# Kernel optimization log

Hardware: AMD Instinct MI355X
Metric: run time of the kernel (lower is better)

## Reference

```python
import jax, jax.numpy as jnp
import numpy as np

EMBED = 768
HEADS = 12
HEAD_DIM = EMBED // HEADS


def setup_inputs() -> dict:
    key = jax.random.key(0)
    ks = jax.random.split(key, 7)
    B, S = 4, 2048
    scale = 1.0 / np.sqrt(EMBED)
    return {
        "q": jax.random.normal(ks[0], (B, S, EMBED), dtype=jnp.float32),
        "k": jax.random.normal(ks[1], (B, S, EMBED), dtype=jnp.float32),
        "v": jax.random.normal(ks[2], (B, S, EMBED), dtype=jnp.float32),
        # NOTE: original torch code applies self.query to q, k AND v (bug kept faithfully),
        # so only the query projection and the output projection participate.
        "Wq": (jax.random.normal(ks[3], (EMBED, EMBED), dtype=jnp.float32) * scale),
        "bq": jnp.zeros((EMBED,), dtype=jnp.float32),
        "Wo": (jax.random.normal(ks[4], (EMBED, EMBED), dtype=jnp.float32) * scale),
        "bo": jnp.zeros((EMBED,), dtype=jnp.float32),
    }


def _split_heads(x):
    B, S, _ = x.shape
    return x.reshape(B, S, HEADS, HEAD_DIM).transpose(0, 2, 1, 3)  # [B,H,S,D]


def reference(q, k, v, Wq, bq, Wo, bo):
    # All three streams go through the *query* projection (faithful to source bug).
    qh = _split_heads(q @ Wq.T + bq)
    kh = _split_heads(k @ Wq.T + bq)
    vh = _split_heads(v @ Wq.T + bq)
    scores = jnp.einsum("bhsd,bhtd->bhst", qh, kh) / np.sqrt(HEAD_DIM)  # [B,H,S,S]
    attn = jax.nn.softmax(scores, axis=-1)  # dropout = identity (eval mode)
    out = jnp.einsum("bhst,bhtd->bhsd", attn, vh)  # [B,H,S,D]
    B, H, S, D = out.shape
    out = out.transpose(0, 2, 1, 3).reshape(B, S, H * D)  # [B,S,E]
    return out @ Wo.T + bo
```

## Files before the change

### kernel.cpp

```cpp
#include <hip/hip_runtime.h>

typedef unsigned int  uint32;
typedef unsigned short ushort_t;

using s16x8 = __attribute__((ext_vector_type(8))) short;
using bf8v  = __attribute__((ext_vector_type(8))) __bf16;
using f16x4 = __attribute__((ext_vector_type(4))) _Float16;
using f16x8 = __attribute__((ext_vector_type(8))) _Float16;
using f32x4 = __attribute__((ext_vector_type(4))) float;

typedef __attribute__((address_space(1))) void as1_void;
typedef __attribute__((address_space(3))) void as3_void;

__device__ __forceinline__ void gld16(const void* g, void* l) {
  __builtin_amdgcn_global_load_lds((const as1_void*)g, (as3_void*)l, 16, 0, 0);
}

__device__ __forceinline__ f32x4 mfma32(s16x8 a, s16x8 b, f32x4 c) {
  return __builtin_amdgcn_mfma_f32_16x16x32_bf16(
      __builtin_bit_cast(bf8v, a), __builtin_bit_cast(bf8v, b), c, 0, 0, 0);
}
__device__ __forceinline__ f32x4 mfma32h(f16x8 a, f16x8 b, f32x4 c) {
  return __builtin_amdgcn_mfma_f32_16x16x32_f16(a, b, c, 0, 0, 0);
}

__device__ __forceinline__ ushort_t f2bf(float f) {
  uint32 u = __float_as_uint(f);
  u += 0x7FFFu + ((u >> 16) & 1u);
  return (ushort_t)(u >> 16);
}
__device__ __forceinline__ f16x4 exp_pack(f32x4 st) {
  float e0 = __builtin_amdgcn_exp2f(st[0]);
  float e1 = __builtin_amdgcn_exp2f(st[1]);
  float e2 = __builtin_amdgcn_exp2f(st[2]);
  float e3 = __builtin_amdgcn_exp2f(st[3]);
  uint2 u = {__builtin_bit_cast(uint32, __builtin_amdgcn_cvt_pkrtz(e0, e1)),
             __builtin_bit_cast(uint32, __builtin_amdgcn_cvt_pkrtz(e2, e3))};
  return __builtin_bit_cast(f16x4, u);
}

__global__ __launch_bounds__(256) void cvt_all(const float* __restrict__ q,
                                               const float* __restrict__ k,
                                               const float* __restrict__ v,
                                               const float* __restrict__ Wq,
                                               const float* __restrict__ Wo,
                                               ushort_t* qb, ushort_t* kb, ushort_t* vb,
                                               ushort_t* wqb, ushort_t* wob) {
  int i = blockIdx.x * 256 + threadIdx.x;
  const float* s; ushort_t* d; int off;
  if (i < 4718592) {
    int st = i / 1572864; off = i - st * 1572864;
    s = st == 0 ? q : (st == 1 ? k : v);
    d = st == 0 ? qb : (st == 1 ? kb : vb);
  } else {
    int j = i - 4718592; int st = j / 147456; off = j - st * 147456;
    s = st ? Wo : Wq; d = st ? wob : wqb;
  }
  float4 f = ((const float4*)s)[off];
  ushort4 o = {f2bf(f.x), f2bf(f.y), f2bf(f.z), f2bf(f.w)};
  ((ushort4*)d)[off] = o;
}

__device__ __forceinline__ void gemm_core(const ushort_t* __restrict__ A,
                                          const ushort_t* __restrict__ Bw,
                                          ushort_t* As, ushort_t* Bs,
                                          int m0, int n0, f32x4 (&acc)[4][4]) {
  const int tid = threadIdx.x;
  const int wave = tid >> 6, lane = tid & 63;
  const int qd = lane >> 4, c = lane & 15;
  const int wm = wave >> 1, wn = wave & 1;
  const int pc0 = qd ^ (c & 7), pc1 = (4 + qd) ^ (c & 7);
  int row[4], cl[4], lb[4];
#pragma unroll
  for (int i = 0; i < 4; ++i) {
    int s = i * 256 + wave * 64 + lane;
    row[i] = s >> 3; cl[i] = (s & 7) ^ (row[i] & 7);
    lb[i] = (i * 256 + wave * 64) * 16;
  }
  for (int kt = 0; kt < 12; ++kt) {
    __syncthreads();
#pragma unroll
    for (int i = 0; i < 4; ++i) {
      gld16(A + (size_t)(m0 + row[i]) * 768 + kt * 64 + cl[i] * 8, (char*)As + lb[i]);
      gld16(Bw + (size_t)(n0 + row[i]) * 768 + kt * 64 + cl[i] * 8, (char*)Bs + lb[i]);
    }
    __syncthreads();
#pragma unroll
    for (int kk = 0; kk < 2; ++kk) {
      const int pcr = kk ? pc1 : pc0;
      s16x8 a[4], b[4];
#pragma unroll
      for (int i = 0; i < 4; ++i) a[i] = *(const s16x8*)(As + (wm * 64 + i * 16 + c) * 64 + pcr * 8);
#pragma unroll
      for (int j = 0; j < 4; ++j) b[j] = *(const s16x8*)(Bs + (wn * 64 + j * 16 + c) * 64 + pcr * 8);
#pragma unroll
      for (int i = 0; i < 4; ++i)
#pragma unroll
        for (int j = 0; j < 4; ++j) acc[i][j] = mfma32(a[i], b[j], acc[i][j]);
    }
  }
}

__global__ __launch_bounds__(256) void gemm_proj(const ushort_t* __restrict__ qb,
                                                 const ushort_t* __restrict__ kb,
                                                 const ushort_t* __restrict__ vb,
                                                 const ushort_t* __restrict__ Wqb,
                                                 const float* __restrict__ bias,
                                                 ushort_t* __restrict__ qh,
                                                 ushort_t* __restrict__ kh,
                                                 ushort_t* __restrict__ vt) {
  __shared__ __align__(16) ushort_t As[8192];
  __shared__ __align__(16) ushort_t Bs[8192];
  const int bz = blockIdx.z;
  const ushort_t* A = bz == 0 ? qb : (bz == 1 ? kb : vb);
  const int m0 = blockIdx.y * 128, n0 = blockIdx.x * 128;
  f32x4 acc[4][4] = {};
  gemm_core(A, Wqb, As, Bs, m0, n0, acc);
  const int tid = threadIdx.x, wave = tid >> 6, lane = tid & 63;
  const int qd = lane >> 4, c = lane & 15;
  const int wm = wave >> 1, wn = wave & 1;
  if (bz == 2) {
    const int sbase = m0 & 2047, bb = m0 >> 11;
#pragma unroll
    for (int p = 0; p < 2; ++p) {
      __syncthreads();
      if (wn == p) {
#pragma unroll
        for (int j = 0; j < 4; ++j) {
          int n64 = j * 16 + c;
          float bv = bias[n0 + p * 64 + n64];
#pragma unroll
          for (int i = 0; i < 4; ++i) {
            int ps8 = (wm * 16 + i * 4 + qd) ^ ((c & 7) << 2);
            uint2 w = {__builtin_bit_cast(uint32, __builtin_amdgcn_cvt_pkrtz(acc[i][j][0] + bv, acc[i][j][1] + bv)),
                       __builtin_bit_cast(uint32, __builtin_amdgcn_cvt_pkrtz(acc[i][j][2] + bv, acc[i][j][3] + bv))};
            *(uint2*)(As + n64 * 128 + ps8 * 4) = w;
          }
        }
      }
      __syncthreads();
      const int h = (n0 >> 6) + p;
#pragma unroll
      for (int e = 0; e < 4; ++e) {
        int ch = e * 256 + tid;
        int n64 = ch >> 4, u = ch & 15;
        uint4 w = *(const uint4*)(As + n64 * 128 + (u ^ ((n64 & 7) << 1)) * 8);
        *(uint4*)(vt + ((size_t)(bb * 12 + h) * 64 + n64) * 2048 + sbase + u * 8) = w;
      }
    }
  } else {
    ushort_t* dst = bz == 0 ? qh : kh;
    const float qsc = bz == 0 ? 0.18033688011112042f : 1.0f;
#pragma unroll
    for (int j = 0; j < 4; ++j) {
      int n = n0 + wn * 64 + j * 16 + c;
      float bv = bias[n];
      int h = n >> 6, d = n & 63;
#pragma unroll
      for (int i = 0; i < 4; ++i)
#pragma unroll
        for (int r = 0; r < 4; ++r) {
          int m = m0 + wm * 64 + i * 16 + qd * 4 + r;
          int bb = m >> 11, s = m & 2047;
          dst[((size_t)((bb * 12 + h) * 2048 + s)) * 64 + d] = f2bf((acc[i][j][r] + bv) * qsc);
        }
    }
  }
}

__global__ __launch_bounds__(256) void gemm_final(const ushort_t* __restrict__ A,
                                                  const ushort_t* __restrict__ Wob,
                                                  const float* __restrict__ bias,
                                                  float* __restrict__ out) {
  __shared__ __align__(16) ushort_t As[4096];
  __shared__ __align__(16) ushort_t Bs[8192];
  const int m0 = blockIdx.y * 64, n0 = blockIdx.x * 128;
  const int tid = threadIdx.x;
  const int wave = tid >> 6, lane = tid & 63;
  const int qd = lane >> 4, c = lane & 15;
  const int wm = wave >> 1, wn = wave & 1;
  const int pc0 = qd ^ (c & 7), pc1 = (4 + qd) ^ (c & 7);
  f32x4 acc[2][4] = {};
  int arow[2], acl[2], alb[2], brow[4], bcl[4], blb[4];
#pragma unroll
  for (int i = 0; i < 2; ++i) {
    int s = i * 256 + tid;
    arow[i] = s >> 3; acl[i] = (s & 7) ^ (arow[i] & 7);
    alb[i] = (i * 256 + wave * 64) * 16;
  }
#pragma unroll
  for (int i = 0; i < 4; ++i) {
    int s = i * 256 + tid;
    brow[i] = s >> 3; bcl[i] = (s & 7) ^ (brow[i] & 7);
    blb[i] = (i * 256 + wave * 64) * 16;
  }
  for (int kt = 0; kt < 12; ++kt) {
    __syncthreads();
#pragma unroll
    for (int i = 0; i < 2; ++i)
      gld16(A + (size_t)(m0 + arow[i]) * 768 + kt * 64 + acl[i] * 8, (char*)As + alb[i]);
#pragma unroll
    for (int i = 0; i < 4; ++i)
      gld16(Wob + (size_t)(n0 + brow[i]) * 768 + kt * 64 + bcl[i] * 8, (char*)Bs + blb[i]);
    __syncthreads();
#pragma unroll
    for (int kk = 0; kk < 2; ++kk) {
      const int pcr = kk ? pc1 : pc0;
      s16x8 a[2], b[4];
#pragma unroll
      for (int i = 0; i < 2; ++i) a[i] = *(const s16x8*)(As + (wm * 32 + i * 16 + c) * 64 + pcr * 8);
#pragma unroll
      for (int j = 0; j < 4; ++j) b[j] = *(const s16x8*)(Bs + (wn * 64 + j * 16 + c) * 64 + pcr * 8);
#pragma unroll
      for (int i = 0; i < 2; ++i)
#pragma unroll
        for (int j = 0; j < 4; ++j) acc[i][j] = mfma32(a[i], b[j], acc[i][j]);
    }
  }
#pragma unroll
  for (int j = 0; j < 4; ++j) {
    int n = n0 + wn * 64 + j * 16 + c;
    float bv = bias[n];
#pragma unroll
    for (int i = 0; i < 2; ++i)
#pragma unroll
      for (int r = 0; r < 4; ++r) {
        int m = m0 + wm * 32 + i * 16 + qd * 4 + r;
        out[(size_t)m * 768 + n] = acc[i][j][r] + bv;
      }
  }
}

__global__ __launch_bounds__(512, 6) void flash(const ushort_t* __restrict__ qh,
                                                const ushort_t* __restrict__ kh,
                                                const ushort_t* __restrict__ vt,
                                                ushort_t* __restrict__ attn) {
  __shared__ __align__(16) ushort_t Ks[128 * 64];
  __shared__ __align__(16) ushort_t Vts[64 * 128];
  const int bid = blockIdx.x;
  const int bh = bid % 48, qt = bid / 48;
  const int tid = threadIdx.x, wave = tid >> 6, lane = tid & 63;
  const int qd = lane >> 4, c = lane & 15;
  const ushort_t* Qg = qh + (size_t)bh * 131072;
  const ushort_t* Kg = kh + (size_t)bh * 131072;
  const ushort_t* Vg = vt + (size_t)bh * 131072;
  const int sb = qt * 128 + wave * 16;

  s16x8 qf[2];
#pragma unroll
  for (int kk = 0; kk < 2; ++kk)
    qf[kk] = *(const s16x8*)(Qg + (size_t)(sb + c) * 64 + kk * 32 + qd * 8);

  const f32x4 z4 = {0.f, 0.f, 0.f, 0.f};
  const float FM = 12.0f;
  const f32x4 nFM = {-FM, -FM, -FM, -FM};
  f32x4 o[4], lacc = z4;
#pragma unroll
  for (int dn = 0; dn < 4; ++dn) o[dn] = z4;
  f16x8 ones8;
#pragma unroll
  for (int e = 0; e < 8; ++e) ones8[e] = (_Float16)1.f;

  const int kpc0 = (qd) ^ (c & 7);
  const int kpc1 = (4 + qd) ^ (c & 7);

  int kgrow[2], kcl[2], vrow[2], vcl[2], lbase[2];
#pragma unroll
  for (int i = 0; i < 2; ++i) {
    int s = i * 512 + tid;
    int kr = s >> 3; kcl[i] = (s & 7) ^ (kr & 7);
    int u = kr & 31;
    kgrow[i] = (kr & ~31) | (((u >> 2) & 3) << 3) | (((u >> 4) & 1) << 2) | (u & 3);
    vrow[i] = s >> 4; vcl[i] = (s & 15) ^ (vrow[i] & 15);
    lbase[i] = (i * 512 + wave * 64) * 16;
  }

  for (int kt = 0; kt < 16; ++kt) {
    __syncthreads();
#pragma unroll
    for (int i = 0; i < 2; ++i)
      gld16(Kg + (size_t)(kt * 128 + kgrow[i]) * 64 + kcl[i] * 8, (char*)Ks + lbase[i]);
#pragma unroll
    for (int i = 0; i < 2; ++i)
      gld16(Vg + (size_t)vrow[i] * 2048 + kt * 128 + vcl[i] * 8, (char*)Vts + lbase[i]);
    __syncthreads();

#pragma unroll
    for (int p = 0; p < 4; ++p) {
      f16x4 p0[2];
#pragma unroll
      for (int tile = 0; tile < 2; ++tile) {
        const int r = (p * 2 + tile) * 16 + c;
        s16x8 a0 = *(const s16x8*)(Ks + r * 64 + kpc0 * 8);
        s16x8 a1 = *(const s16x8*)(Ks + r * 64 + kpc1 * 8);
        __builtin_amdgcn_s_setprio(1);
        f32x4 st0 = mfma32(a0, qf[0], nFM);
        st0 = mfma32(a1, qf[1], st0);
        __builtin_amdgcn_s_setprio(0);
        p0[tile] = exp_pack(st0);
      }
      f16x8 A0 = __builtin_shufflevector(p0[0], p0[1], 0, 1, 2, 3, 4, 5, 6, 7);
      __builtin_amdgcn_s_setprio(1);
      lacc = mfma32h(A0, ones8, lacc);
#pragma unroll
      for (int dn = 0; dn < 4; ++dn) {
        f16x8 vb = *(const f16x8*)(Vts + (dn * 16 + c) * 128 + ((4 * p + qd) ^ c) * 8);
        o[dn] = mfma32h(A0, vb, o[dn]);
      }
      __builtin_amdgcn_s_setprio(0);
    }
  }

  const int bb = bh / 12, h = bh % 12;
#pragma unroll
  for (int r = 0; r < 4; ++r) {
    float inv = 1.f / lacc[r];
    int s = sb + qd * 4 + r;
#pragma unroll
    for (int dn = 0; dn < 4; ++dn) {
      float val = o[dn][r] * inv;
      attn[((size_t)(bb * 2048 + s)) * 768 + h * 64 + dn * 16 + c] = f2bf(val);
    }
  }
}

extern "C" void kernel_launch(void* const* d_in, const int* in_sizes, int n_in,
                              void* d_out, int out_size, void* d_ws, size_t ws_size,
                              hipStream_t stream) {
  const float* q  = (const float*)d_in[0];
  const float* k  = (const float*)d_in[1];
  const float* v  = (const float*)d_in[2];
  const float* Wq = (const float*)d_in[3];
  const float* bq = (const float*)d_in[4];
  const float* Wo = (const float*)d_in[5];
  const float* bo = (const float*)d_in[6];
  float* out = (float*)d_out;
  char* ws = (char*)d_ws;

  ushort_t* qbf = (ushort_t*)(ws + 0);
  ushort_t* kbf = (ushort_t*)(ws + 12582912);
  ushort_t* vbf = (ushort_t*)(ws + 25165824);
  ushort_t* wqb = (ushort_t*)(ws + 37748736);
  ushort_t* wob = (ushort_t*)(ws + 38928384);
  ushort_t* qhp = (ushort_t*)(ws + 40108032);
  ushort_t* khp = (ushort_t*)(ws + 52690944);
  ushort_t* vtp = (ushort_t*)(ws + 65273856);
  ushort_t* att = (ushort_t*)(ws + 0);

  cvt_all<<<dim3(19584), 256, 0, stream>>>(q, k, v, Wq, Wo, qbf, kbf, vbf, wqb, wob);
  gemm_proj<<<dim3(6, 64, 3), 256, 0, stream>>>(qbf, kbf, vbf, wqb, bq, qhp, khp, vtp);
  flash<<<dim3(768), 512, 0, stream>>>(qhp, khp, vtp, att);
  gemm_final<<<dim3(6, 128), 256, 0, stream>>>(att, wob, bo, out);
}
```

Measured before the change: 251.6 us.

## Split key tile across wave pairs, each wave handling two query sub-tiles

Each wave now owns 32 query rows (two 16-row sub-tiles) and half of every 128-key tile, instead of 16 query rows over the whole key tile. Each K and V fragment read from LDS is therefore reused for two query sub-tiles, halving LDS reads per MFMA. Partial output and row-sum accumulators from the two key-half waves are combined through shared memory at the end. The cost is doubled accumulator registers per wave, which may reduce occupancy under the 512x6 launch bounds, plus an extra reduction with added barriers.

Result: slower. 429.3 us (+70.6%).

```diff
diff --git a/kernel.cpp b/kernel.cpp
--- a/kernel.cpp
+++ b/kernel.cpp
@@ -240,29 +240,37 @@
   const int bid = blockIdx.x;
   const int bh = bid % 48, qt = bid / 48;
   const int tid = threadIdx.x, wave = tid >> 6, lane = tid & 63;
+  const int wq = wave >> 1, wk = wave & 1;
   const int qd = lane >> 4, c = lane & 15;
   const ushort_t* Qg = qh + (size_t)bh * 131072;
   const ushort_t* Kg = kh + (size_t)bh * 131072;
   const ushort_t* Vg = vt + (size_t)bh * 131072;
-  const int sb = qt * 128 + wave * 16;
-
-  s16x8 qf[2];
-#pragma unroll
-  for (int kk = 0; kk < 2; ++kk)
-    qf[kk] = *(const s16x8*)(Qg + (size_t)(sb + c) * 64 + kk * 32 + qd * 8);
+  const int sb = qt * 128 + wq * 32;
+
+  s16x8 qf[2][2];
+#pragma unroll
+  for (int ts = 0; ts < 2; ++ts)
+#pragma unroll
+    for (int kk = 0; kk < 2; ++kk)
+      qf[ts][kk] = *(const s16x8*)(Qg + (size_t)(sb + ts * 16 + c) * 64 + kk * 32 + qd * 8);
 
   const f32x4 z4 = {0.f, 0.f, 0.f, 0.f};
   const float FM = 12.0f;
   const f32x4 nFM = {-FM, -FM, -FM, -FM};
-  f32x4 o[4], lacc = z4;
-#pragma unroll
-  for (int dn = 0; dn < 4; ++dn) o[dn] = z4;
+  f32x4 o[2][4], lacc[2];
+#pragma unroll
+  for (int ts = 0; ts < 2; ++ts) {
+    lacc[ts] = z4;
+#pragma unroll
+    for (int dn = 0; dn < 4; ++dn) o[ts][dn] = z4;
+  }
   f16x8 ones8;
 #pragma unroll
   for (int e = 0; e < 8; ++e) ones8[e] = (_Float16)1.f;
 
   const int kpc0 = (qd) ^ (c & 7);
   const int kpc1 = (4 + qd) ^ (c & 7);
+  const int pbase = wk * 2;
 
   int kgrow[2], kcl[2], vrow[2], vcl[2], lbase[2];
 #pragma unroll
@@ -286,40 +294,67 @@
     __syncthreads();
 
 #pragma unroll
-    for (int p = 0; p < 4; ++p) {
-      f16x4 p0[2];
+    for (int pp = 0; pp < 2; ++pp) {
+      const int p = pbase + pp;
+      f16x4 e0[2], e1[2];
 #pragma unroll
       for (int tile = 0; tile < 2; ++tile) {
         const int r = (p * 2 + tile) * 16 + c;
         s16x8 a0 = *(const s16x8*)(Ks + r * 64 + kpc0 * 8);
         s16x8 a1 = *(const s16x8*)(Ks + r * 64 + kpc1 * 8);
         __builtin_amdgcn_s_setprio(1);
-        f32x4 st0 = mfma32(a0, qf[0], nFM);
-        st0 = mfma32(a1, qf[1], st0);
+        f32x4 st0 = mfma32(a0, qf[0][0], nFM);
+        f32x4 st1 = mfma32(a0, qf[1][0], nFM);
+        st0 = mfma32(a1, qf[0][1], st0);
+        st1 = mfma32(a1, qf[1][1], st1);
         __builtin_amdgcn_s_setprio(0);
-        p0[tile] = exp_pack(st0);
-      }
-      f16x8 A0 = __builtin_shufflevector(p0[0], p0[1], 0, 1, 2, 3, 4, 5, 6, 7);
+        e0[tile] = exp_pack(st0);
+        e1[tile] = exp_pack(st1);
+      }
+      f16x8 A0 = __builtin_shufflevector(e0[0], e0[1], 0, 1, 2, 3, 4, 5, 6, 7);
+      f16x8 A1 = __builtin_shufflevector(e1[0], e1[1], 0, 1, 2, 3, 4, 5, 6, 7);
       __builtin_amdgcn_s_setprio(1);
-      lacc = mfma32h(A0, ones8, lacc);
+      lacc[0] = mfma32h(A0, ones8, lacc[0]);
+      lacc[1] = mfma32h(A1, ones8, lacc[1]);
 #pragma unroll
       for (int dn = 0; dn < 4; ++dn) {
         f16x8 vb = *(const f16x8*)(Vts + (dn * 16 + c) * 128 + ((4 * p + qd) ^ c) * 8);
-        o[dn] = mfma32h(A0, vb, o[dn]);
+        o[0][dn] = mfma32h(A0, vb, o[0][dn]);
+        o[1][dn] = mfma32h(A1, vb, o[1][dn]);
       }
       __builtin_amdgcn_s_setprio(0);
     }
   }
 
+  float* red = (float*)Ks;
+  const int rbase = (wq * 64 + lane) * 21;
   const int bb = bh / 12, h = bh % 12;
 #pragma unroll
-  for (int r = 0; r < 4; ++r) {
-    float inv = 1.f / lacc[r];
-    int s = sb + qd * 4 + r;
-#pragma unroll
-    for (int dn = 0; dn < 4; ++dn) {
-      float val = o[dn][r] * inv;
-      attn[((size_t)(bb * 2048 + s)) * 768 + h * 64 + dn * 16 + c] = f2bf(val);
+  for (int ts = 0; ts < 2; ++ts) {
+    __syncthreads();
+    if (wk == 1) {
+#pragma unroll
+      for (int dn = 0; dn < 4; ++dn)
+#pragma unroll
+        for (int r = 0; r < 4; ++r) red[rbase + dn * 4 + r] = o[ts][dn][r];
+#pragma unroll
+      for (int r = 0; r < 4; ++r) red[rbase + 16 + r] = lacc[ts][r];
+    }
+    __syncthreads();
+    if (wk == 0) {
+      float l4[4];
+#pragma unroll
+      for (int r = 0; r < 4; ++r) l4[r] = lacc[ts][r] + red[rbase + 16 + r];
+#pragma unroll
+      for (int r = 0; r < 4; ++r) {
+        float inv = 1.f / l4[r];
+        int s = sb + ts * 16 + qd * 4 + r;
+#pragma unroll
+        for (int dn = 0; dn < 4; ++dn) {
+          float val = (o[ts][dn][r] + red[rbase + dn * 4 + r]) * inv;
+          attn[((size_t)(bb * 2048 + s)) * 768 + h * 64 + dn * 16 + c] = f2bf(val);
+        }
+      }
     }
   }
 }
```
